# Optimization experiments

Hardware: AMD Instinct MI355X
Metric: run time of the kernel (lower is better)

Reference implementation:

```python
import jax, jax.numpy as jnp
import numpy as np

D_MODEL = 2048
N_Q_HEADS = 32
N_KV_HEADS = 8
HEAD_DIM = D_MODEL // N_Q_HEADS  # 64
KV_DIM = HEAD_DIM * N_KV_HEADS   # 512
B, S = 2, 2048


def setup_inputs() -> dict:
    key = jax.random.key(0)
    ks = jax.random.split(key, 11)
    sc_d = 1.0 / np.sqrt(D_MODEL)
    return {
        "query": jax.random.normal(ks[0], (B, S, D_MODEL), jnp.float32),
        "key":   jax.random.normal(ks[1], (B, S, D_MODEL), jnp.float32),
        "value": jax.random.normal(ks[2], (B, S, D_MODEL), jnp.float32),
        "Wq": jax.random.normal(ks[3], (D_MODEL, D_MODEL), jnp.float32) * sc_d,
        "bq": jnp.zeros((D_MODEL,), jnp.float32),
        "Wk": jax.random.normal(ks[4], (D_MODEL, KV_DIM), jnp.float32) * sc_d,
        "bk": jnp.zeros((KV_DIM,), jnp.float32),
        "Wv": jax.random.normal(ks[5], (D_MODEL, KV_DIM), jnp.float32) * sc_d,
        "bv": jnp.zeros((KV_DIM,), jnp.float32),
        "Wo": jax.random.normal(ks[6], (D_MODEL, D_MODEL), jnp.float32) * sc_d,
        "bo": jnp.zeros((D_MODEL,), jnp.float32),
    }


def reference(query, key, value, Wq, bq, Wk, bk, Wv, bv, Wo, bo):
    b, s, _ = query.shape
    g = N_Q_HEADS // N_KV_HEADS  # num groups
    # projections
    Q = query @ Wq + bq                      # [b, s, d_model]
    K = key @ Wk + bk                        # [b, s, kv_dim]
    V = value @ Wv + bv                      # [b, s, kv_dim]
    # split heads. Torch code splits Q into groups of num_kv_heads heads,
    # and each group broadcasts per-head against the Hkv KV heads, i.e.
    # query head (grp*Hkv + j) attends against kv head j.
    Q = Q.reshape(b, s, g, N_KV_HEADS, HEAD_DIM)  # [b, s, g, hkv, d]
    K = K.reshape(b, s, N_KV_HEADS, HEAD_DIM)     # [b, s, hkv, d]
    V = V.reshape(b, s, N_KV_HEADS, HEAD_DIM)
    scale = 1.0 / jnp.sqrt(jnp.float32(HEAD_DIM))
    scores = jnp.einsum('bsghd,bthd->bghst', Q, K) * scale  # [b,g,hkv,s,s]
    attn = jax.nn.softmax(scores, axis=-1)
    out = jnp.einsum('bghst,bthd->bsghd', attn, V)          # [b,s,g,hkv,d]
    # concat over groups then heads == original head order (g major, hkv minor)
    out = out.reshape(b, s, D_MODEL)
    return out @ Wo + bo
```

## Files before the change

kernel.cpp:

```cpp
#include <hip/hip_runtime.h>
#include <cstdint>

typedef _Float16 half4 __attribute__((ext_vector_type(4)));
typedef _Float16 half8 __attribute__((ext_vector_type(8)));
typedef _Float16 half16 __attribute__((ext_vector_type(16)));
typedef float f32x4 __attribute__((ext_vector_type(4)));
typedef float f32x16 __attribute__((ext_vector_type(16)));

#define L2E 1.44269504088896340736f

__device__ __forceinline__ void gl16(const void* g, void* l) {
  __builtin_amdgcn_global_load_lds(
      (const __attribute__((address_space(1))) void*)g,
      (__attribute__((address_space(3))) void*)l, 16, 0, 0);
}

__device__ __forceinline__ uint32_t pk2(float a, float b) {
  return __builtin_bit_cast(uint32_t, __builtin_amdgcn_cvt_pkrtz(a, b));
}

__device__ __forceinline__ void plswap(uint32_t& x, uint32_t& y) {
  auto r = __builtin_amdgcn_permlane32_swap((int)x, (int)y, false, false);
  x = (uint32_t)r[0];
  y = (uint32_t)r[1];
}

__device__ __forceinline__ f32x16 zero16() {
  f32x16 z;
  #pragma unroll
  for (int r = 0; r < 16; ++r) z[r] = 0.0f;
  return z;
}

__global__ __launch_bounds__(256) void cvt_f32_f16_3(
    const float* __restrict__ s0, const float* __restrict__ s1, const float* __restrict__ s2,
    _Float16* __restrict__ d0, _Float16* __restrict__ d1, _Float16* __restrict__ d2)
{
  const float* src = (blockIdx.z == 0) ? s0 : (blockIdx.z == 1 ? s1 : s2);
  _Float16* dst    = (blockIdx.z == 0) ? d0 : (blockIdx.z == 1 ? d1 : d2);
  size_t i = ((size_t)blockIdx.x * 256 + threadIdx.x) * 8;
  float4 a = *(const float4*)(src + i);
  float4 b = *(const float4*)(src + i + 4);
  half8 o;
  o[0] = (_Float16)a.x; o[1] = (_Float16)a.y; o[2] = (_Float16)a.z; o[3] = (_Float16)a.w;
  o[4] = (_Float16)b.x; o[5] = (_Float16)b.y; o[6] = (_Float16)b.z; o[7] = (_Float16)b.w;
  *(half8*)(dst + i) = o;
}

__global__ __launch_bounds__(256) void transpose_w_all(
    const float* __restrict__ Wq, const float* __restrict__ Wk,
    const float* __restrict__ Wv, const float* __restrict__ Wo,
    _Float16* __restrict__ WqkvT, _Float16* __restrict__ WoT)
{
  int id = blockIdx.x;
  const float* src;
  _Float16* dst;
  int N, tx, ty;
  if (id < 4096)      { src = Wq; dst = WqkvT;                        N = 2048; tx = id & 63; ty = id >> 6; }
  else if (id < 5120) { id -= 4096; src = Wk; dst = WqkvT + (size_t)2048 * 2048; N = 512; tx = id & 15; ty = id >> 4; }
  else if (id < 6144) { id -= 5120; src = Wv; dst = WqkvT + (size_t)2560 * 2048; N = 512; tx = id & 15; ty = id >> 4; }
  else                { id -= 6144; src = Wo; dst = WoT;              N = 2048; tx = id & 63; ty = id >> 6; }
  const int n0 = tx * 32, k0 = ty * 32;
  __shared__ float t[32][33];
  #pragma unroll
  for (int i = 0; i < 4; ++i)
    t[threadIdx.y + i * 8][threadIdx.x] =
        src[(size_t)(k0 + threadIdx.y + i * 8) * N + n0 + threadIdx.x];
  __syncthreads();
  #pragma unroll
  for (int i = 0; i < 4; ++i)
    dst[(size_t)(n0 + threadIdx.y + i * 8) * 2048 + k0 + threadIdx.x] =
        (_Float16)t[threadIdx.x][threadIdx.y + i * 8];
}

__global__ __launch_bounds__(256) void transpose_v(
    const _Float16* __restrict__ QKV, _Float16* __restrict__ VT)
{
  const int bh = blockIdx.z;
  const int bb = bh >> 3, h = bh & 7;
  const int t0 = blockIdx.x * 32, d0 = blockIdx.y * 32;
  __shared__ _Float16 t[32][33];
  const _Float16* src = QKV + (size_t)(bb * 2048) * 3072 + 2560 + h * 64;
  #pragma unroll
  for (int i = 0; i < 4; ++i)
    t[threadIdx.y + i * 8][threadIdx.x] =
        src[(size_t)(t0 + threadIdx.y + i * 8) * 3072 + d0 + threadIdx.x];
  __syncthreads();
  _Float16* dst = VT + ((size_t)(bb * 8 + h) * 64) * 2048;
  #pragma unroll
  for (int i = 0; i < 4; ++i)
    dst[(size_t)(d0 + threadIdx.y + i * 8) * 2048 + t0 + threadIdx.x] =
        t[threadIdx.x][threadIdx.y + i * 8];
}

template<int MODE>
__global__ __launch_bounds__(256) void gemm_f16(
    const _Float16* __restrict__ Aq, const _Float16* __restrict__ Ak, const _Float16* __restrict__ Av,
    const _Float16* __restrict__ Bt,
    const float* __restrict__ bias0, const float* __restrict__ bias1, const float* __restrict__ bias2,
    _Float16* __restrict__ Ch, float* __restrict__ Cf, const int K, const int N)
{
  const int m0 = blockIdx.x * 128;
  const int n0 = blockIdx.y * 128;
  const _Float16* A = Aq;
  if constexpr (MODE == 0) { if (n0 >= 2560) A = Av; else if (n0 >= 2048) A = Ak; }
  const int tid = threadIdx.x;
  const int lane = tid & 63;
  const int w = tid >> 6;
  const int wr = w >> 1, wc = w & 1;
  const int lo = lane & 15, hi = lane >> 4;

  __shared__ __align__(1024) _Float16 Asm[128 * 64];
  __shared__ __align__(1024) _Float16 Bsm[128 * 64];

  f32x4 acc[4][4];
  #pragma unroll
  for (int i = 0; i < 4; ++i)
    #pragma unroll
    for (int j = 0; j < 4; ++j)
      acc[i][j] = (f32x4){0.f, 0.f, 0.f, 0.f};

  const int li = lane >> 3;
  const int lc = lane & 7;
  const int kslot = lc ^ li;
  const _Float16* Asrc = A  + (size_t)(m0 + w * 32 + li) * K + kslot * 8;
  const _Float16* Bsrc = Bt + (size_t)(n0 + w * 32 + li) * K + kslot * 8;
  char* Adst = (char*)Asm + w * 4096;
  char* Bdst = (char*)Bsm + w * 4096;

  for (int k0 = 0; k0 < K; k0 += 64) {
    __syncthreads();
    #pragma unroll
    for (int u = 0; u < 4; ++u) {
      gl16(Asrc + k0 + (size_t)u * 8 * K, Adst + u * 1024);
      gl16(Bsrc + k0 + (size_t)u * 8 * K, Bdst + u * 1024);
    }
    __syncthreads();
    #pragma unroll
    for (int kp = 0; kp < 2; ++kp) {
      half8 af[4], bf[4];
      #pragma unroll
      for (int i = 0; i < 4; ++i) {
        const int ra = wr * 64 + i * 16 + lo;
        af[i] = *(const half8*)((const char*)Asm + ra * 128 + ((kp * 64 + hi * 16) ^ ((ra & 7) << 4)));
        const int rb = wc * 64 + i * 16 + lo;
        bf[i] = *(const half8*)((const char*)Bsm + rb * 128 + ((kp * 64 + hi * 16) ^ ((rb & 7) << 4)));
      }
      #pragma unroll
      for (int i = 0; i < 4; ++i)
        #pragma unroll
        for (int j = 0; j < 4; ++j)
          acc[i][j] = __builtin_amdgcn_mfma_f32_16x16x32_f16(af[i], bf[j], acc[i][j], 0, 0, 0);
    }
  }

  float* T = (float*)Asm;
  const int tr = tid >> 3;
  const int slot = tid & 7;
  #pragma unroll
  for (int i = 0; i < 4; ++i) {
    __syncthreads();
    #pragma unroll
    for (int j = 0; j < 4; ++j)
      #pragma unroll
      for (int r = 0; r < 4; ++r)
        T[(wr * 16 + 4 * hi + r) * 128 + wc * 64 + j * 16 + lo] = acc[i][j][r];
    __syncthreads();
    const int grow = m0 + (tr >> 4) * 64 + i * 16 + (tr & 15);
    const int gcol = n0 + slot * 16;
    const float* Trow = T + tr * 128 + slot * 16;
    float4 v[4];
    #pragma unroll
    for (int q = 0; q < 4; ++q) v[q] = ((const float4*)Trow)[q];
    const float* bp = bias0;
    int cb = gcol;
    if constexpr (MODE == 0) {
      if (gcol >= 2560) { bp = bias2; cb = gcol - 2560; }
      else if (gcol >= 2048) { bp = bias1; cb = gcol - 2048; }
    }
    float4 bvv[4];
    #pragma unroll
    for (int q = 0; q < 4; ++q) bvv[q] = ((const float4*)(bp + cb))[q];
    if constexpr (MODE == 0) {
      half16 o;
      #pragma unroll
      for (int q = 0; q < 4; ++q) {
        o[4 * q + 0] = (_Float16)(v[q].x + bvv[q].x);
        o[4 * q + 1] = (_Float16)(v[q].y + bvv[q].y);
        o[4 * q + 2] = (_Float16)(v[q].z + bvv[q].z);
        o[4 * q + 3] = (_Float16)(v[q].w + bvv[q].w);
      }
      *(half16*)(Ch + (size_t)grow * N + gcol) = o;
    } else {
      float* dst = Cf + (size_t)grow * N + gcol;
      #pragma unroll
      for (int q = 0; q < 4; ++q) {
        float4 ov = {v[q].x + bvv[q].x, v[q].y + bvv[q].y, v[q].z + bvv[q].z, v[q].w + bvv[q].w};
        ((float4*)dst)[q] = ov;
      }
    }
  }
}

__global__ __launch_bounds__(256, 4) void attn_fwd4(
    const _Float16* __restrict__ QKV, const _Float16* __restrict__ VT,
    _Float16* __restrict__ AO)
{
  const int wg = blockIdx.x;
  const int work = (wg & 7) * 128 + (wg >> 3);
  const int bh = work >> 6;
  const int b = bh >> 3, h = bh & 7;
  const int rem = work & 63;
  const int qh = (rem >> 4) * 8 + h;
  const int qt = rem & 15;

  const int tid = threadIdx.x;
  const int lane = tid & 63;
  const int w = tid >> 6;
  const int l31 = lane & 31;
  const int hi5 = lane >> 5;
  const int r7 = l31 & 7;

  __shared__ __align__(1024) char sm[2][2][8192];

  const _Float16 QSC = (_Float16)(0.125f * L2E);
  const int qrow0 = b * 2048 + qt * 128 + w * 32 + l31;
  half8 qf[4];
  {
    const _Float16* qp = QKV + (size_t)qrow0 * 3072 + qh * 64 + hi5 * 8;
    #pragma unroll
    for (int s = 0; s < 4; ++s) {
      half8 q = *(const half8*)(qp + s * 16);
      #pragma unroll
      for (int e = 0; e < 8; ++e) q[e] = q[e] * QSC;
      qf[s] = q;
    }
  }

  const int li = lane >> 3;
  const int lc = lane & 7;
  const int kslot = lc ^ li;
  const int w16li = w * 16 + li;
  const _Float16* Ksrc = QKV + ((size_t)(b * 2048 + w16li)) * 3072 + 2048 + h * 64 + kslot * 8;
  const _Float16* Vsrc = VT + ((size_t)(b * 8 + h) * 64 + w16li) * 2048 + kslot * 8;

  f32x16 oa[2];
  oa[0] = zero16();
  oa[1] = zero16();
  float lreg = 0.f;

  {
    char* kd = &sm[0][0][0] + w * 2048;
    char* vd = &sm[0][1][0] + w * 2048;
    gl16(Ksrc, kd);
    gl16(Ksrc + (size_t)8 * 3072, kd + 1024);
    gl16(Vsrc, vd);
    gl16(Vsrc + (size_t)8 * 2048, vd + 1024);
  }
  __syncthreads();

  int cur = 0;
  for (int t = 0; t < 32; ++t) {
    if (t < 31) {
      const int t0 = (t + 1) * 64;
      char* kd = &sm[cur ^ 1][0][0] + w * 2048;
      char* vd = &sm[cur ^ 1][1][0] + w * 2048;
      const _Float16* kg = Ksrc + (size_t)t0 * 3072;
      const _Float16* vg = Vsrc + t0;
      gl16(kg, kd);
      gl16(kg + (size_t)8 * 3072, kd + 1024);
      gl16(vg, vd);
      gl16(vg + (size_t)8 * 2048, vd + 1024);
    }

    const char* Kb = &sm[cur][0][0];
    const char* Vb = &sm[cur][1][0];

    uint32_t pw[4][4];
    float ps = 0.f;
    #pragma unroll
    for (int j = 0; j < 2; ++j) {
      f32x16 sa = zero16();
      const int kr = j * 32 + l31;
      __builtin_amdgcn_s_setprio(1);
      #pragma unroll
      for (int s = 0; s < 4; ++s) {
        half8 kf = *(const half8*)(Kb + kr * 128 + (((2 * s + hi5) ^ r7) << 4));
        sa = __builtin_amdgcn_mfma_f32_32x32x16_f16(kf, qf[s], sa, 0, 0, 0);
      }
      __builtin_amdgcn_s_setprio(0);
      #pragma unroll
      for (int r = 0; r < 16; ++r) {
        const float p = __builtin_amdgcn_exp2f(sa[r]);
        sa[r] = p;
        ps += p;
      }
      #pragma unroll
      for (int hf = 0; hf < 2; ++hf) {
        const int rb = hf * 8;
        uint32_t w0 = pk2(sa[rb + 0], sa[rb + 1]);
        uint32_t w1 = pk2(sa[rb + 2], sa[rb + 3]);
        uint32_t w2 = pk2(sa[rb + 4], sa[rb + 5]);
        uint32_t w3 = pk2(sa[rb + 6], sa[rb + 7]);
        plswap(w0, w2);
        plswap(w1, w3);
        const int s = 2 * j + hf;
        pw[s][0] = w0; pw[s][1] = w1; pw[s][2] = w2; pw[s][3] = w3;
      }
    }
    ps += __shfl_xor(ps, 32);
    lreg += ps;

    __builtin_amdgcn_s_setprio(1);
    #pragma unroll
    for (int s = 0; s < 4; ++s) {
      union { uint32_t u[4]; half8 h; } p0;
      #pragma unroll
      for (int u = 0; u < 4; ++u) p0.u[u] = pw[s][u];
      #pragma unroll
      for (int i = 0; i < 2; ++i) {
        const int vr = i * 32 + l31;
        half8 vf = *(const half8*)(Vb + vr * 128 + (((2 * s + hi5) ^ r7) << 4));
        oa[i] = __builtin_amdgcn_mfma_f32_32x32x16_f16(vf, p0.h, oa[i], 0, 0, 0);
      }
    }
    __builtin_amdgcn_s_setprio(0);

    __syncthreads();
    cur ^= 1;
  }

  {
    const float inv = 1.0f / lreg;
    #pragma unroll
    for (int i = 0; i < 2; ++i) {
      _Float16* dst = AO + (size_t)qrow0 * 2048 + qh * 64 + i * 32 + hi5 * 4;
      #pragma unroll
      for (int q = 0; q < 4; ++q) {
        union { uint32_t u[2]; half4 h4; } o;
        o.u[0] = pk2(oa[i][4 * q + 0] * inv, oa[i][4 * q + 1] * inv);
        o.u[1] = pk2(oa[i][4 * q + 2] * inv, oa[i][4 * q + 3] * inv);
        *(half4*)(dst + 8 * q) = o.h4;
      }
    }
  }
}

extern "C" void kernel_launch(void* const* d_in, const int* in_sizes, int n_in,
                              void* d_out, int out_size, void* d_ws, size_t ws_size,
                              hipStream_t stream) {
  const float* query = (const float*)d_in[0];
  const float* key   = (const float*)d_in[1];
  const float* value = (const float*)d_in[2];
  const float* Wq = (const float*)d_in[3];
  const float* bq = (const float*)d_in[4];
  const float* Wk = (const float*)d_in[5];
  const float* bk = (const float*)d_in[6];
  const float* Wv = (const float*)d_in[7];
  const float* bv = (const float*)d_in[8];
  const float* Wo = (const float*)d_in[9];
  const float* bo = (const float*)d_in[10];
  float* out = (float*)d_out;

  char* ws = (char*)d_ws;
  _Float16* qh    = (_Float16*)(ws);
  _Float16* kh    = (_Float16*)(ws + 16777216);
  _Float16* vh    = (_Float16*)(ws + 33554432);
  _Float16* WqkvT = (_Float16*)(ws + 50331648);
  _Float16* WoT   = (_Float16*)(ws + 62914560);
  _Float16* QKVh  = (_Float16*)(ws + 71303168);
  _Float16* VT    = (_Float16*)(ws + 96468992);
  _Float16* aoh   = (_Float16*)(ws + 100663296);

  cvt_f32_f16_3<<<dim3(4096, 1, 3), 256, 0, stream>>>(query, key, value, qh, kh, vh);
  transpose_w_all<<<10240, dim3(32, 8), 0, stream>>>(Wq, Wk, Wv, Wo, WqkvT, WoT);
  gemm_f16<0><<<dim3(32, 24), 256, 0, stream>>>(qh, kh, vh, WqkvT, bq, bk, bv,
                                                QKVh, nullptr, 2048, 3072);
  transpose_v<<<dim3(64, 2, 16), dim3(32, 8), 0, stream>>>(QKVh, VT);
  attn_fwd4<<<1024, 256, 0, stream>>>(QKVh, VT, aoh);
  gemm_f16<1><<<dim3(32, 16), 256, 0, stream>>>(aoh, nullptr, nullptr, WoT, bo,
                                                nullptr, nullptr, nullptr, out, 2048, 2048);
}
```

Baseline: 265.7 us.

## Replace GEMMs with 256x256-tile triple-buffered pipelined kernel

Replaces the 128x128 single-stage GEMM with a 512-thread kernel that computes 256x256 output tiles. It uses a three-stage LDS ring with K-step 32 and vmcnt-based waits, so global-to-LDS loads overlap the MFMA work. It also adds an XCD-aware workgroup remap and raises wave priority around the MFMAs. The larger tiles cut redundant global loads per FLOP, but the grids shrink to 192 and 128 workgroups, which leaves many CUs idle. The LDS layout also drops the XOR swizzle, which may cause bank conflicts.

Measured after the change: 260.9 us. No clear change (-1.8%).

```diff
diff --git a/kernel.cpp b/kernel.cpp
--- a/kernel.cpp
+++ b/kernel.cpp
@@ -94,81 +94,107 @@
 }
 
 template<int MODE>
-__global__ __launch_bounds__(256) void gemm_f16(
+__global__ __launch_bounds__(512, 2) void gemm256(
     const _Float16* __restrict__ Aq, const _Float16* __restrict__ Ak, const _Float16* __restrict__ Av,
     const _Float16* __restrict__ Bt,
     const float* __restrict__ bias0, const float* __restrict__ bias1, const float* __restrict__ bias2,
-    _Float16* __restrict__ Ch, float* __restrict__ Cf, const int K, const int N)
+    _Float16* __restrict__ Ch, float* __restrict__ Cf)
 {
-  const int m0 = blockIdx.x * 128;
-  const int n0 = blockIdx.y * 128;
+  constexpr int K = 2048;
+  constexpr int N = (MODE == 0) ? 3072 : 2048;
+  constexpr int NB = N / 256;
+  constexpr int G = 16 * NB;
+
+  const int wg = blockIdx.x;
+  const int work = (wg & 7) * (G / 8) + (wg >> 3);
+  const int m0 = (work / NB) * 256;
+  const int n0 = (work % NB) * 256;
+
   const _Float16* A = Aq;
   if constexpr (MODE == 0) { if (n0 >= 2560) A = Av; else if (n0 >= 2048) A = Ak; }
+
   const int tid = threadIdx.x;
   const int lane = tid & 63;
   const int w = tid >> 6;
-  const int wr = w >> 1, wc = w & 1;
+  const int wr = w >> 2;
+  const int wc = w & 3;
   const int lo = lane & 15, hi = lane >> 4;
 
-  __shared__ __align__(1024) _Float16 Asm[128 * 64];
-  __shared__ __align__(1024) _Float16 Bsm[128 * 64];
-
-  f32x4 acc[4][4];
-  #pragma unroll
-  for (int i = 0; i < 4; ++i)
-    #pragma unroll
-    for (int j = 0; j < 4; ++j)
-      acc[i][j] = (f32x4){0.f, 0.f, 0.f, 0.f};
-
-  const int li = lane >> 3;
-  const int lc = lane & 7;
-  const int kslot = lc ^ li;
-  const _Float16* Asrc = A  + (size_t)(m0 + w * 32 + li) * K + kslot * 8;
-  const _Float16* Bsrc = Bt + (size_t)(n0 + w * 32 + li) * K + kslot * 8;
-  char* Adst = (char*)Asm + w * 4096;
-  char* Bdst = (char*)Bsm + w * 4096;
-
-  for (int k0 = 0; k0 < K; k0 += 64) {
+  __shared__ __align__(1024) char smem[98304];
+
+  f32x4 acc[8][4];
+  #pragma unroll
+  for (int mt = 0; mt < 8; ++mt)
+    #pragma unroll
+    for (int nt = 0; nt < 4; ++nt)
+      acc[mt][nt] = (f32x4){0.f, 0.f, 0.f, 0.f};
+
+  const int srow = lane >> 2;
+  const int sslot = lane & 3;
+  const _Float16* pA = A  + (size_t)(m0 + w * 32 + srow) * K + sslot * 8;
+  const _Float16* pB = Bt + (size_t)(n0 + w * 32 + srow) * K + sslot * 8;
+  const size_t rstep = (size_t)16 * K;
+  const int dst = w * 2048;
+
+  {
+    char* b0 = smem;
+    char* b1 = smem + 32768;
+    gl16(pA,            b0 + dst);          gl16(pA + rstep,            b0 + dst + 1024);
+    gl16(pB,            b0 + 16384 + dst);  gl16(pB + rstep,            b0 + 16384 + dst + 1024);
+    gl16(pA + 32,       b1 + dst);          gl16(pA + 32 + rstep,       b1 + dst + 1024);
+    gl16(pB + 32,       b1 + 16384 + dst);  gl16(pB + 32 + rstep,       b1 + 16384 + dst + 1024);
+  }
+  pA += 64; pB += 64;
+  asm volatile("s_waitcnt vmcnt(4)" ::: "memory");
+  __builtin_amdgcn_s_barrier();
+
+  const int abase = (wr * 128 + lo) * 64 + hi * 16;
+  const int bbase = 16384 + (wc * 64 + lo) * 64 + hi * 16;
+
+  int c = 0;
+  for (int t = 0; t < 64; ++t) {
+    int c1 = c + 1; if (c1 == 3) c1 = 0;
+    int c2 = c1 + 1; if (c2 == 3) c2 = 0;
+    if (t < 62) {
+      char* bp = smem + (c2 << 15);
+      gl16(pA,         bp + dst);          gl16(pA + rstep,         bp + dst + 1024);
+      gl16(pB,         bp + 16384 + dst);  gl16(pB + rstep,         bp + 16384 + dst + 1024);
+      pA += 32; pB += 32;
+    }
+    const char* bc = smem + (c << 15);
+    half8 af[8], bf[4];
+    #pragma unroll
+    for (int mt = 0; mt < 8; ++mt) af[mt] = *(const half8*)(bc + abase + mt * 1024);
+    #pragma unroll
+    for (int nt = 0; nt < 4; ++nt) bf[nt] = *(const half8*)(bc + bbase + nt * 1024);
+    __builtin_amdgcn_s_setprio(1);
+    #pragma unroll
+    for (int mt = 0; mt < 8; ++mt)
+      #pragma unroll
+      for (int nt = 0; nt < 4; ++nt)
+        acc[mt][nt] = __builtin_amdgcn_mfma_f32_16x16x32_f16(af[mt], bf[nt], acc[mt][nt], 0, 0, 0);
+    __builtin_amdgcn_s_setprio(0);
+    if (t < 62)       asm volatile("s_waitcnt vmcnt(4)" ::: "memory");
+    else if (t == 62) asm volatile("s_waitcnt vmcnt(0)" ::: "memory");
+    if (t < 63) __builtin_amdgcn_s_barrier();
+    c = c1;
+  }
+
+  float* T = (float*)smem;
+  const int tr = tid >> 4;
+  const int sc = tid & 15;
+  #pragma unroll
+  for (int mp = 0; mp < 8; ++mp) {
     __syncthreads();
     #pragma unroll
-    for (int u = 0; u < 4; ++u) {
-      gl16(Asrc + k0 + (size_t)u * 8 * K, Adst + u * 1024);
-      gl16(Bsrc + k0 + (size_t)u * 8 * K, Bdst + u * 1024);
-    }
+    for (int nt = 0; nt < 4; ++nt)
+      #pragma unroll
+      for (int r = 0; r < 4; ++r)
+        T[(wr * 16 + 4 * hi + r) * 256 + wc * 64 + nt * 16 + lo] = acc[mp][nt][r];
     __syncthreads();
-    #pragma unroll
-    for (int kp = 0; kp < 2; ++kp) {
-      half8 af[4], bf[4];
-      #pragma unroll
-      for (int i = 0; i < 4; ++i) {
-        const int ra = wr * 64 + i * 16 + lo;
-        af[i] = *(const half8*)((const char*)Asm + ra * 128 + ((kp * 64 + hi * 16) ^ ((ra & 7) << 4)));
-        const int rb = wc * 64 + i * 16 + lo;
-        bf[i] = *(const half8*)((const char*)Bsm + rb * 128 + ((kp * 64 + hi * 16) ^ ((rb & 7) << 4)));
-      }
-      #pragma unroll
-      for (int i = 0; i < 4; ++i)
-        #pragma unroll
-        for (int j = 0; j < 4; ++j)
-          acc[i][j] = __builtin_amdgcn_mfma_f32_16x16x32_f16(af[i], bf[j], acc[i][j], 0, 0, 0);
-    }
-  }
-
-  float* T = (float*)Asm;
-  const int tr = tid >> 3;
-  const int slot = tid & 7;
-  #pragma unroll
-  for (int i = 0; i < 4; ++i) {
-    __syncthreads();
-    #pragma unroll
-    for (int j = 0; j < 4; ++j)
-      #pragma unroll
-      for (int r = 0; r < 4; ++r)
-        T[(wr * 16 + 4 * hi + r) * 128 + wc * 64 + j * 16 + lo] = acc[i][j][r];
-    __syncthreads();
-    const int grow = m0 + (tr >> 4) * 64 + i * 16 + (tr & 15);
-    const int gcol = n0 + slot * 16;
-    const float* Trow = T + tr * 128 + slot * 16;
+    const int grow = m0 + (tr >> 4) * 128 + mp * 16 + (tr & 15);
+    const int gcol = n0 + sc * 16;
+    const float* Trow = T + tr * 256 + sc * 16;
     float4 v[4];
     #pragma unroll
     for (int q = 0; q < 4; ++q) v[q] = ((const float4*)Trow)[q];
@@ -192,11 +218,11 @@
       }
       *(half16*)(Ch + (size_t)grow * N + gcol) = o;
     } else {
-      float* dst = Cf + (size_t)grow * N + gcol;
+      float* dstp = Cf + (size_t)grow * N + gcol;
       #pragma unroll
       for (int q = 0; q < 4; ++q) {
         float4 ov = {v[q].x + bvv[q].x, v[q].y + bvv[q].y, v[q].z + bvv[q].z, v[q].w + bvv[q].w};
-        ((float4*)dst)[q] = ov;
+        ((float4*)dstp)[q] = ov;
       }
     }
   }
@@ -374,10 +400,8 @@
 
   cvt_f32_f16_3<<<dim3(4096, 1, 3), 256, 0, stream>>>(query, key, value, qh, kh, vh);
   transpose_w_all<<<10240, dim3(32, 8), 0, stream>>>(Wq, Wk, Wv, Wo, WqkvT, WoT);
-  gemm_f16<0><<<dim3(32, 24), 256, 0, stream>>>(qh, kh, vh, WqkvT, bq, bk, bv,
-                                                QKVh, nullptr, 2048, 3072);
+  gemm256<0><<<192, 512, 0, stream>>>(qh, kh, vh, WqkvT, bq, bk, bv, QKVh, nullptr);
   transpose_v<<<dim3(64, 2, 16), dim3(32, 8), 0, stream>>>(QKVh, VT);
   attn_fwd4<<<1024, 256, 0, stream>>>(QKVh, VT, aoh);
-  gemm_f16<1><<<dim3(32, 16), 256, 0, stream>>>(aoh, nullptr, nullptr, WoT, bo,
-                                                nullptr, nullptr, nullptr, out, 2048, 2048);
-}
+  gemm256<1><<<128, 512, 0, stream>>>(aoh, nullptr, nullptr, WoT, bo, nullptr, nullptr, nullptr, out);
+}
```
